# Performance work log

Measured on AMD Instinct MI355X. Metric: run time of the kernel, lower is better.

## Reference

```python
import jax, jax.numpy as jnp
import numpy as np

EPS = 1e-6

def _ln(x):
    mu = jnp.mean(x, -1, keepdims=True)
    var = jnp.mean((x - mu) ** 2, -1, keepdims=True)
    return (x - mu) / jnp.sqrt(var + EPS)

def _mha(q_in, k_in, v_in, w, mask, h):
    # w: [4, d, d] = (Wq, Wk, Wv, Wo), stored as [in, out]
    b, sq, d = q_in.shape
    dk = d // h
    q = (q_in @ w[0]).reshape(b, sq, h, dk)
    k = (k_in @ w[1]).reshape(b, k_in.shape[1], h, dk)
    v = (v_in @ w[2]).reshape(b, v_in.shape[1], h, dk)
    scores = jnp.einsum('bqhd,bkhd->bhqk', q, k) / np.sqrt(dk).astype(q.dtype)
    if mask is not None:
        scores = jnp.where(mask, scores, jnp.asarray(-jnp.inf, scores.dtype))
    attn = jax.nn.softmax(scores, -1)
    out = jnp.einsum('bhqk,bkhd->bqhd', attn, v).reshape(b, sq, d)
    return out @ w[3]

def setup_inputs() -> dict:
    B, S, D, V, NL, ML = 8, 256, 1024, 32000, 6, 256
    ks = jax.random.split(jax.random.key(0), 8)
    sc = 0.02
    return {
        'memory': jax.random.normal(ks[0], (B, S, D), jnp.float32),
        'gold_tokens': jax.random.randint(ks[1], (B, ML), 0, V),
        'attn_w': jax.random.normal(ks[2], (NL, 2, 4, D, D), jnp.float32) * sc,
        'ffn_w1': jax.random.normal(ks[3], (NL, D, 4 * D), jnp.float32) * sc,
        'ffn_w2': jax.random.normal(ks[4], (NL, 4 * D, D), jnp.float32) * sc,
        'tok_emb': jax.random.normal(ks[5], (V, D - ML), jnp.float32) * sc,
        'sos': jax.random.normal(ks[6], (D,), jnp.float32),
        'gen_w': jax.random.normal(ks[7], (D, V), jnp.float32) * sc,
    }

def reference(memory, gold_tokens, attn_w, ffn_w1, ffn_w2, tok_emb, sos, gen_w):
    B = memory.shape[0]
    ML = gold_tokens.shape[1]          # max_length == decoder len
    NL = attn_w.shape[0]
    H = 8
    temperature = 1.0
    # embedding: token embed (dim d-ML) concat one-hot position (dim ML)
    dec_input = gold_tokens[:, :-1]                      # [B, ML-1]
    tok = tok_emb[dec_input]                             # [B, ML-1, D-ML]
    pos = jax.nn.one_hot(jnp.arange(ML - 1), ML, dtype=tok.dtype)  # [ML-1, ML]
    pos = jnp.broadcast_to(pos[None], (B, ML - 1, ML))
    emb = jnp.concatenate([tok, pos], -1)                # [B, ML-1, D]
    sos_tok = jnp.broadcast_to(sos[None, None, :], (B, 1, sos.shape[0]))
    x = jnp.concatenate([sos_tok, emb], 1)               # [B, ML, D]
    causal = jnp.tril(jnp.ones((ML, ML), bool))[None, None]  # True = keep
    for l in range(NL):
        h1 = _ln(x)
        x = x + _mha(h1, h1, h1, attn_w[l, 0], causal, H)       # self-attn
        x = x + _mha(_ln(x), memory, memory, attn_w[l, 1], None, H)  # cross-attn (raw memory keys/values)
        h2 = _ln(x)
        x = x + jax.nn.relu(h2 @ ffn_w1[l]) @ ffn_w2[l]
    logits = _ln(x) @ gen_w
    return jax.nn.log_softmax(logits / temperature, -1)
```

## Files before the change

### kernel.cpp

```cpp
#include <hip/hip_runtime.h>
#include <hip/hip_bf16.h>
#include <cstdint>
#include <cstddef>

using bf16 = __hip_bfloat16;
typedef __attribute__((ext_vector_type(8))) short bf16x8;
typedef __attribute__((ext_vector_type(4))) float f32x4;

#define DEV static __device__ __forceinline__

DEV unsigned short f2bf(float f) {
    bf16 h = __float2bfloat16(f);
    return __builtin_bit_cast(unsigned short, h);
}

typedef const __attribute__((address_space(1))) void* as1cv;
typedef __attribute__((address_space(3))) void* as3v;

DEV void load_lds16(const void* g, void* l) {
    __builtin_amdgcn_global_load_lds((as1cv)g, (as3v)l, 16, 0, 0);
}

template<int EPI>
__global__ __launch_bounds__(256)
void gemm_k(const bf16* __restrict__ Ag, const bf16* __restrict__ Bg,
            void* __restrict__ Cg,
            int Mdim, int Ndim, int Kdim,
            int lda, int ldb, int ldc,
            int Hdim, long aZ1, long aZ2, long bZ1, long bZ2,
            long cZ1, long cZ2, float scale,
            float* __restrict__ pp, const bf16* __restrict__ Ag2, int ySplitA)
{
    __shared__ __align__(16) char lds[65536];

    const int t = threadIdx.x;
    const int wave = t >> 6, lane = t & 63;
    const int wr = wave >> 1, wc = wave & 1;
    const int lo = lane & 15, hi = lane >> 4;

    const int bx2 = blockIdx.x, by2 = blockIdx.y;
    const int m0 = bx2 * 128, n0 = by2 * 128;
    const int z = blockIdx.z;
    const int z1 = z / Hdim, z2 = z - z1 * Hdim;

    const bf16* Abase = (by2 >= ySplitA) ? Ag2 : Ag;
    const bf16* A = Abase + (size_t)z1 * aZ1 + (size_t)z2 * aZ2;
    const bf16* B = Bg + (size_t)z1 * bZ1 + (size_t)z2 * bZ2;

    f32x4 acc[4][4];
#pragma unroll
    for (int m = 0; m < 4; ++m)
#pragma unroll
        for (int n = 0; n < 4; ++n)
            acc[m][n] = f32x4{0.f, 0.f, 0.f, 0.f};

    const int nk = Kdim >> 6;

    auto stage = [&](int kt, int buf) {
        const int k0 = kt << 6;
        char* dA = lds + buf * 32768;
        char* dB = dA + 16384;
#pragma unroll
        for (int i = 0; i < 4; ++i) {
            int u = i * 256 + t;
            int row = u >> 3;
            int cb = (u & 7) ^ (row & 7);
            load_lds16(A + (size_t)(m0 + row) * lda + (k0 + cb * 8),
                       dA + i * 4096 + wave * 1024);
        }
#pragma unroll
        for (int i = 0; i < 4; ++i) {
            int u = i * 256 + t;
            int row = u >> 3;
            int cb = (u & 7) ^ (row & 7);
            load_lds16(B + (size_t)(n0 + row) * ldb + (k0 + cb * 8),
                       dB + i * 4096 + wave * 1024);
        }
    };

    stage(0, 0);
    int cur = 0;
    for (int kt = 0; kt < nk; ++kt) {
        __syncthreads();
        if (kt + 1 < nk) stage(kt + 1, cur ^ 1);
        char* ldsA = lds + cur * 32768;
        char* ldsB = ldsA + 16384;
#pragma unroll
        for (int kk = 0; kk < 2; ++kk) {
            bf16x8 af[4], bfr[4];
#pragma unroll
            for (int m = 0; m < 4; ++m) {
                int row = wr * 64 + m * 16 + lo;
                int cbyte = ((kk << 6) + (hi << 4)) ^ ((row & 7) << 4);
                af[m] = *(const bf16x8*)(ldsA + row * 128 + cbyte);
            }
#pragma unroll
            for (int n = 0; n < 4; ++n) {
                int row = wc * 64 + n * 16 + lo;
                int cbyte = ((kk << 6) + (hi << 4)) ^ ((row & 7) << 4);
                bfr[n] = *(const bf16x8*)(ldsB + row * 128 + cbyte);
            }
#pragma unroll
            for (int m = 0; m < 4; ++m)
#pragma unroll
                for (int n = 0; n < 4; ++n)
                    acc[m][n] = __builtin_amdgcn_mfma_f32_16x16x32_bf16(
                        af[m], bfr[n], acc[m][n], 0, 0, 0);
        }
        cur ^= 1;
    }

    const int rb = hi << 2;
    if (EPI == 0 || EPI == 1) {
        unsigned short* C = (unsigned short*)Cg + (size_t)z1 * cZ1 + (size_t)z2 * cZ2;
#pragma unroll
        for (int m = 0; m < 4; ++m)
#pragma unroll
            for (int n = 0; n < 4; ++n)
#pragma unroll
                for (int r = 0; r < 4; ++r) {
                    int row = m0 + wr * 64 + m * 16 + rb + r;
                    int col = n0 + wc * 64 + n * 16 + lo;
                    float v = acc[m][n][r];
                    if (EPI == 1) v = fmaxf(v, 0.f);
                    C[(size_t)row * ldc + col] = f2bf(v);
                }
    } else {
        float* C = (float*)Cg + (size_t)z1 * cZ1 + (size_t)z2 * cZ2;
#pragma unroll
        for (int m = 0; m < 4; ++m)
#pragma unroll
            for (int n = 0; n < 4; ++n)
#pragma unroll
                for (int r = 0; r < 4; ++r) {
                    int row = m0 + wr * 64 + m * 16 + rb + r;
                    int col = n0 + wc * 64 + n * 16 + lo;
                    atomicAdd(&C[(size_t)row * ldc + col], acc[m][n][r]);
                }
    }
}

__global__ __launch_bounds__(512, 2)
void gemm256_k(const bf16* __restrict__ Ag, const bf16* __restrict__ Bg,
               float* __restrict__ Cg, int Kdim, int lda, int ldb, int ldc,
               float* __restrict__ pp)
{
    __shared__ __align__(16) char lds[98304];

    const int t = threadIdx.x;
    const int wave = t >> 6, lane = t & 63;
    const int wr = wave >> 2, wc = wave & 3;
    const int lo = lane & 15, hi = lane >> 4;
    const int m0 = blockIdx.x * 256, n0 = blockIdx.y * 256;

    f32x4 acc[8][4];
#pragma unroll
    for (int m = 0; m < 8; ++m)
#pragma unroll
        for (int n = 0; n < 4; ++n)
            acc[m][n] = f32x4{0.f, 0.f, 0.f, 0.f};

    const int NT = Kdim >> 5;

    auto stageOp = [&](const bf16* Op, int ld, int base0, int kt, char* dst) {
#pragma unroll
        for (int i = 0; i < 2; ++i) {
            int u = i * 512 + t;
            int row = u >> 2, j = u & 3;
            int cb = j ^ (row & 3);
            load_lds16(Op + (size_t)(base0 + row) * ld + (kt << 5) + cb * 8,
                       dst + i * 8192 + wave * 1024);
        }
    };

    stageOp(Ag, lda, m0, 0, lds);
    stageOp(Bg, ldb, n0, 0, lds + 16384);
    stageOp(Ag, lda, m0, 1, lds + 32768);
    stageOp(Bg, ldb, n0, 1, lds + 32768 + 16384);

    for (int kt = 0; kt < NT; ++kt) {
        if (kt == NT - 1) asm volatile("s_waitcnt vmcnt(0)" ::: "memory");
        else              asm volatile("s_waitcnt vmcnt(4)" ::: "memory");
        __builtin_amdgcn_s_barrier();
        __builtin_amdgcn_sched_barrier(0);

        char* cA = lds + (kt % 3) * 32768;
        char* cB = cA + 16384;
        char* nA = lds + ((kt + 2) % 3) * 32768;

        if (kt + 2 < NT) stageOp(Ag, lda, m0, kt + 2, nA);
        bf16x8 bfr[4];
#pragma unroll
        for (int nf = 0; nf < 4; ++nf) {
            int rb_ = wc * 64 + nf * 16 + lo;
            bfr[nf] = *(const bf16x8*)(cB + rb_ * 64 + ((hi ^ (rb_ & 3)) << 4));
        }
        bf16x8 af[4];
#pragma unroll
        for (int mm = 0; mm < 4; ++mm) {
            int ra = wr * 128 + mm * 16 + lo;
            af[mm] = *(const bf16x8*)(cA + ra * 64 + ((hi ^ (ra & 3)) << 4));
        }
        __builtin_amdgcn_s_setprio(1);
#pragma unroll
        for (int mm = 0; mm < 4; ++mm)
#pragma unroll
            for (int nf = 0; nf < 4; ++nf)
                acc[mm][nf] = __builtin_amdgcn_mfma_f32_16x16x32_bf16(
                    af[mm], bfr[nf], acc[mm][nf], 0, 0, 0);
        __builtin_amdgcn_s_setprio(0);

        if (kt + 2 < NT) stageOp(Bg, ldb, n0, kt + 2, nA + 16384);
#pragma unroll
        for (int mm = 0; mm < 4; ++mm) {
            int ra = wr * 128 + (4 + mm) * 16 + lo;
            af[mm] = *(const bf16x8*)(cA + ra * 64 + ((hi ^ (ra & 3)) << 4));
        }
        __builtin_amdgcn_s_setprio(1);
#pragma unroll
        for (int mm = 0; mm < 4; ++mm)
#pragma unroll
            for (int nf = 0; nf < 4; ++nf)
                acc[4 + mm][nf] = __builtin_amdgcn_mfma_f32_16x16x32_bf16(
                    af[mm], bfr[nf], acc[4 + mm][nf], 0, 0, 0);
        __builtin_amdgcn_s_setprio(0);
    }

#pragma unroll
    for (int mf = 0; mf < 8; ++mf)
#pragma unroll
        for (int nf = 0; nf < 4; ++nf)
#pragma unroll
            for (int r = 0; r < 4; ++r) {
                int row = m0 + wr * 128 + mf * 16 + hi * 4 + r;
                int col = n0 + wc * 64 + nf * 16 + lo;
                __builtin_nontemporal_store(acc[mf][nf][r],
                                            &Cg[(size_t)row * ldc + col]);
            }
    __syncthreads();
    float* lp = (float*)lds;
#pragma unroll
    for (int mf = 0; mf < 8; ++mf)
#pragma unroll
        for (int r = 0; r < 4; ++r) {
            float vm = fmaxf(fmaxf(acc[mf][0][r], acc[mf][1][r]),
                             fmaxf(acc[mf][2][r], acc[mf][3][r]));
#pragma unroll
            for (int o = 1; o < 16; o <<= 1) vm = fmaxf(vm, __shfl_xor(vm, o));
            float vs = 0.f;
#pragma unroll
            for (int nf = 0; nf < 4; ++nf) vs += __expf(acc[mf][nf][r] - vm);
#pragma unroll
            for (int o = 1; o < 16; o <<= 1) vs += __shfl_xor(vs, o);
            if (lo == 0) {
                int rl = wr * 128 + mf * 16 + hi * 4 + r;
                lp[(rl * 4 + wc) * 2 + 0] = vm;
                lp[(rl * 4 + wc) * 2 + 1] = vs;
            }
        }
    __syncthreads();
    if (t < 256) {
        float mm = -3.4e38f, ss = 0.f;
#pragma unroll
        for (int w2 = 0; w2 < 4; ++w2) {
            float m2 = lp[(t * 4 + w2) * 2], s2 = lp[(t * 4 + w2) * 2 + 1];
            float nm = fmaxf(mm, m2);
            ss = ss * __expf(mm - nm) + s2 * __expf(m2 - nm);
            mm = nm;
        }
        size_t idx2 = ((size_t)(m0 + t) * gridDim.y + blockIdx.y) * 2;
        pp[idx2] = mm; pp[idx2 + 1] = ss;
    }
}

template<int CAUSAL>
__global__ __launch_bounds__(256)
void attn_k(const bf16* __restrict__ qkv, const bf16* __restrict__ VT,
            bf16* __restrict__ attno)
{
    __shared__ __align__(16) char ldsK[2][16384];
    __shared__ __align__(16) char ldsP[8192];
    const float SC = 0.088388347648318447f;

    const int t = threadIdx.x, w = t >> 6, lane = t & 63;
    const int lo = lane & 15, hi = lane >> 4;
    const int qb = blockIdx.x, z = blockIdx.y;
    const int b = z >> 3, h = z & 7;
    const int qr0 = qb * 64 + w * 16;

    const unsigned short* Qg = (const unsigned short*)qkv + (size_t)(b * 256) * 3072 + h * 128;
    const unsigned short* Kg = Qg + 1024;
    const unsigned short* VTz = (const unsigned short*)VT + (size_t)z * 32768;

    bf16x8 qf[4];
#pragma unroll
    for (int ks = 0; ks < 4; ++ks)
        qf[ks] = *(const bf16x8*)(Qg + (size_t)(qr0 + lo) * 3072 + ks * 32 + hi * 8);

    f32x4 accO[8];
#pragma unroll
    for (int n2 = 0; n2 < 8; ++n2) accO[n2] = f32x4{0.f, 0.f, 0.f, 0.f};
    float mrun[4], lrun[4];
#pragma unroll
    for (int r = 0; r < 4; ++r) { mrun[r] = -3.0e38f; lrun[r] = 0.f; }

    auto stageK = [&](int kt, int buf) {
#pragma unroll
        for (int i = 0; i < 4; ++i) {
            int u = i * 256 + t;
            int row = u >> 4, j = u & 15;
            int sj = (j & 8) | ((j ^ row) & 7);
            load_lds16(Kg + (size_t)(kt * 64 + row) * 3072 + sj * 8,
                       ldsK[buf] + i * 4096 + w * 1024);
        }
    };

    const int nkt = CAUSAL ? (qb + 1) : 4;
    stageK(0, 0);
    int cur = 0;
    for (int kt = 0; kt < nkt; ++kt) {
        __syncthreads();
        if (kt + 1 < nkt) stageK(kt + 1, cur ^ 1);

        f32x4 s4[4];
#pragma unroll
        for (int n = 0; n < 4; ++n) s4[n] = f32x4{0.f, 0.f, 0.f, 0.f};
#pragma unroll
        for (int ks = 0; ks < 4; ++ks)
#pragma unroll
            for (int n = 0; n < 4; ++n) {
                int kr = n * 16 + lo;
                int c = ks * 4 + hi;
                int sc2 = (c & 8) | ((c ^ (kr & 7)) & 7);
                bf16x8 kf = *(const bf16x8*)(ldsK[cur] + kr * 256 + sc2 * 16);
                s4[n] = __builtin_amdgcn_mfma_f32_16x16x32_bf16(qf[ks], kf, s4[n], 0, 0, 0);
            }

        float sv[4][4];
#pragma unroll
        for (int n = 0; n < 4; ++n)
#pragma unroll
            for (int r = 0; r < 4; ++r) {
                float v = s4[n][r] * SC;
                if (CAUSAL) {
                    int kg = kt * 64 + n * 16 + lo;
                    int qg2 = qb * 64 + w * 16 + hi * 4 + r;
                    if (kg > qg2) v = -3.0e38f;
                }
                sv[n][r] = v;
            }

        float sfv[4];
#pragma unroll
        for (int r = 0; r < 4; ++r) {
            float m2 = fmaxf(fmaxf(sv[0][r], sv[1][r]), fmaxf(sv[2][r], sv[3][r]));
#pragma unroll
            for (int o = 1; o < 16; o <<= 1) m2 = fmaxf(m2, __shfl_xor(m2, o));
            float mn = fmaxf(mrun[r], m2);
            sfv[r] = __expf(mrun[r] - mn);
            mrun[r] = mn;
        }
        float p[4][4], ts[4];
#pragma unroll
        for (int r = 0; r < 4; ++r) ts[r] = 0.f;
#pragma unroll
        for (int n = 0; n < 4; ++n)
#pragma unroll
            for (int r = 0; r < 4; ++r) {
                float e = __expf(sv[n][r] - mrun[r]);
                p[n][r] = e; ts[r] += e;
            }
#pragma unroll
        for (int r = 0; r < 4; ++r) {
            float s2 = ts[r];
#pragma unroll
            for (int o = 1; o < 16; o <<= 1) s2 += __shfl_xor(s2, o);
            lrun[r] = lrun[r] * sfv[r] + s2;
        }
#pragma unroll
        for (int n2 = 0; n2 < 8; ++n2)
#pragma unroll
            for (int r = 0; r < 4; ++r) accO[n2][r] *= sfv[r];

        char* pb = ldsP + w * 2048;
#pragma unroll
        for (int n = 0; n < 4; ++n)
#pragma unroll
            for (int r = 0; r < 4; ++r) {
                int q = hi * 4 + r, k = n * 16 + lo;
                int ch = (k >> 3) ^ (q & 7);
                *(unsigned short*)(pb + q * 128 + ch * 16 + (k & 7) * 2) = f2bf(p[n][r]);
            }

#pragma unroll
        for (int ks2 = 0; ks2 < 2; ++ks2) {
            int c2 = (ks2 * 4 + hi) ^ (lo & 7);
            bf16x8 pa = *(const bf16x8*)(pb + lo * 128 + c2 * 16);
#pragma unroll
            for (int n2 = 0; n2 < 8; ++n2) {
                int d = n2 * 16 + lo;
                bf16x8 vb = *(const bf16x8*)(VTz + (size_t)d * 256 + kt * 64 + ks2 * 32 + hi * 8);
                accO[n2] = __builtin_amdgcn_mfma_f32_16x16x32_bf16(pa, vb, accO[n2], 0, 0, 0);
            }
        }
        cur ^= 1;
    }

    float inv[4];
#pragma unroll
    for (int r = 0; r < 4; ++r) inv[r] = 1.f / lrun[r];
    unsigned short* Og = (unsigned short*)attno;
#pragma unroll
    for (int n2 = 0; n2 < 8; ++n2)
#pragma unroll
        for (int r = 0; r < 4; ++r) {
            int qg2 = qb * 64 + w * 16 + hi * 4 + r;
            int d = n2 * 16 + lo;
            Og[(size_t)(b * 256 + qg2) * 1024 + h * 128 + d] = f2bf(accO[n2][r] * inv[r]);
        }
}

DEV void wconv_tile(const float* __restrict__ W, unsigned short* __restrict__ WT,
                    int K, int N, int k0, int n0, int t, unsigned short* lds)
{
#pragma unroll
    for (int i = 0; i < 16; ++i) {
        int lin = i * 256 + t;
        int r = lin >> 6, c = lin & 63;
        float v = __builtin_nontemporal_load(&W[(size_t)(k0 + r) * N + n0 + c]);
        lds[c * 65 + r] = f2bf(v);
    }
    __syncthreads();
#pragma unroll
    for (int i = 0; i < 16; ++i) {
        int lin = i * 256 + t;
        int r = lin >> 6, c = lin & 63;
        WT[(size_t)(n0 + r) * K + k0 + c] = lds[r * 65 + c];
    }
}

__global__ __launch_bounds__(256)
void wconv_k(const float* __restrict__ W, bf16* __restrict__ WT, int K, int N)
{
    __shared__ unsigned short lds[64 * 65];
    size_t moff = (size_t)blockIdx.z * K * N;
    wconv_tile(W + moff, (unsigned short*)WT + moff, K, N,
               blockIdx.x * 64, blockIdx.y * 64, threadIdx.x, lds);
}

__global__ __launch_bounds__(256)
void wconv3_k(const float* __restrict__ Wa, const float* __restrict__ W1,
              const float* __restrict__ W2, bf16* __restrict__ WTa,
              bf16* __restrict__ WT1, bf16* __restrict__ WT2)
{
    __shared__ unsigned short lds[64 * 65];
    int bid = blockIdx.x, t = threadIdx.x;
    if (bid < 2048) {
        int mat = bid >> 8, r = bid & 255;
        size_t moff = (size_t)mat * 1048576;
        wconv_tile(Wa + moff, (unsigned short*)WTa + moff, 1024, 1024,
                   (r & 15) * 64, (r >> 4) * 64, t, lds);
    } else if (bid < 3072) {
        int idx = bid - 2048;
        wconv_tile(W1, (unsigned short*)WT1, 1024, 4096,
                   (idx & 15) * 64, (idx >> 4) * 64, t, lds);
    } else {
        int idx = bid - 3072;
        wconv_tile(W2, (unsigned short*)WT2, 4096, 1024,
                   (idx & 63) * 64, (idx >> 6) * 64, t, lds);
    }
}

__global__ __launch_bounds__(256)
void f2b_k(const float* __restrict__ in, bf16* __restrict__ out, int n4)
{
    int i = blockIdx.x * 256 + threadIdx.x;
    if (i >= n4) return;
    float4 v = ((const float4*)in)[i];
    ushort4 o;
    o.x = f2bf(v.x); o.y = f2bf(v.y); o.z = f2bf(v.z); o.w = f2bf(v.w);
    ((ushort4*)out)[i] = o;
}

__global__ __launch_bounds__(256)
void embed_k(const float* __restrict__ tok_emb, const int* __restrict__ gold,
             const float* __restrict__ sos, float* __restrict__ x)
{
    int row = blockIdx.x;
    int b = row >> 8, sq = row & 255;
    int c4 = threadIdx.x;
    float4 v;
    if (sq == 0) {
        v = ((const float4*)sos)[c4];
    } else {
        int c = c4 << 2;
        if (c < 768) {
            int tok = gold[b * 256 + sq - 1];
            v = ((const float4*)(tok_emb + (size_t)tok * 768))[c4];
        } else {
            int p = sq - 1;
            v.x = (c + 0 - 768 == p) ? 1.f : 0.f;
            v.y = (c + 1 - 768 == p) ? 1.f : 0.f;
            v.z = (c + 2 - 768 == p) ? 1.f : 0.f;
            v.w = (c + 3 - 768 == p) ? 1.f : 0.f;
        }
    }
    ((float4*)(x + (size_t)row * 1024))[c4] = v;
}

__global__ __launch_bounds__(256)
void ln_k(const float* __restrict__ x, bf16* __restrict__ out)
{
    int row = blockIdx.x;
    const float4* xr = (const float4*)(x + (size_t)row * 1024);
    float4 v = xr[threadIdx.x];
    float s = v.x + v.y + v.z + v.w;
    float ss = v.x * v.x + v.y * v.y + v.z * v.z + v.w * v.w;
    for (int o = 32; o > 0; o >>= 1) { s += __shfl_down(s, o); ss += __shfl_down(ss, o); }
    __shared__ float buf[8];
    int wv = threadIdx.x >> 6;
    if ((threadIdx.x & 63) == 0) { buf[wv] = s; buf[4 + wv] = ss; }
    __syncthreads();
    float S = buf[0] + buf[1] + buf[2] + buf[3];
    float SS = buf[4] + buf[5] + buf[6] + buf[7];
    float mean = S * (1.f / 1024.f);
    float var = SS * (1.f / 1024.f) - mean * mean;
    float rstd = rsqrtf(var + 1e-6f);
    ushort4 o;
    o.x = f2bf((v.x - mean) * rstd);
    o.y = f2bf((v.y - mean) * rstd);
    o.z = f2bf((v.z - mean) * rstd);
    o.w = f2bf((v.w - mean) * rstd);
    ((ushort4*)out)[(size_t)row * 256 + threadIdx.x] = o;
}

__global__ __launch_bounds__(256)
void vtrans_k(const bf16* __restrict__ v, bf16* __restrict__ VT)
{
    __shared__ unsigned short lds[128 * 65];
    int z = blockIdx.y;
    int b = z >> 3, hh = z & 7;
    int sc = blockIdx.x;
    const unsigned short* src = (const unsigned short*)v
        + (size_t)(b * 256 + sc * 64) * 3072 + hh * 128;
    int t = threadIdx.x;
#pragma unroll
    for (int i = 0; i < 32; ++i) {
        int lin = i * 256 + t;
        int sl = lin >> 7, d = lin & 127;
        lds[d * 65 + sl] = src[(size_t)sl * 3072 + d];
    }
    __syncthreads();
    unsigned short* dst = (unsigned short*)VT + (size_t)z * 32768 + sc * 64;
#pragma unroll
    for (int i = 0; i < 32; ++i) {
        int lin = i * 256 + t;
        int d = lin >> 6, sl = lin & 63;
        dst[(size_t)d * 256 + sl] = lds[d * 65 + sl];
    }
}

__global__ __launch_bounds__(256)
void lsesub_k(float* __restrict__ out, const float* __restrict__ pp)
{
    const int NB = 125;
    int row = blockIdx.x, t = threadIdx.x;
    float m = -3.4e38f, s = 0.f;
    if (t < NB) {
        m = pp[((size_t)row * NB + t) * 2];
        s = pp[((size_t)row * NB + t) * 2 + 1];
    }
    for (int o = 32; o > 0; o >>= 1) {
        float om = __shfl_down(m, o), os = __shfl_down(s, o);
        float nm = fmaxf(m, om);
        s = s * __expf(m - nm) + os * __expf(om - nm);
        m = nm;
    }
    __shared__ float bm[4], bs[4];
    __shared__ float sL;
    int wv = t >> 6;
    if ((t & 63) == 0) { bm[wv] = m; bs[wv] = s; }
    __syncthreads();
    if (t == 0) {
        float M = fmaxf(fmaxf(bm[0], bm[1]), fmaxf(bm[2], bm[3]));
        float S = bs[0] * __expf(bm[0] - M) + bs[1] * __expf(bm[1] - M)
                + bs[2] * __expf(bm[2] - M) + bs[3] * __expf(bm[3] - M);
        sL = M + logf(S);
    }
    __syncthreads();
    float L = sL;
    f32x4* p = (f32x4*)(out + (size_t)row * 32000);
    for (int i = t; i < 8000; i += 256) {
        f32x4 v = __builtin_nontemporal_load(&p[i]);
        v[0] -= L; v[1] -= L; v[2] -= L; v[3] -= L;
        __builtin_nontemporal_store(v, &p[i]);
    }
}

extern "C" void kernel_launch(void* const* d_in, const int* in_sizes, int n_in,
                              void* d_out, int out_size, void* d_ws, size_t ws_size,
                              hipStream_t stream)
{
    (void)in_sizes; (void)n_in; (void)out_size;
    const float* memory  = (const float*)d_in[0];
    const int*   gold    = (const int*)d_in[1];
    const float* attn_w  = (const float*)d_in[2];
    const float* ffn_w1  = (const float*)d_in[3];
    const float* ffn_w2  = (const float*)d_in[4];
    const float* tok_emb = (const float*)d_in[5];
    const float* sos     = (const float*)d_in[6];
    const float* gen_w   = (const float*)d_in[7];
    float* out = (float*)d_out;

    char* ws = (char*)d_ws;
    const size_t o_attnW = 0;
    const size_t o_ffn1W = o_attnW + 16777216;
    const size_t o_ffn2W = o_ffn1W + 8388608;
    const size_t o_qkv   = o_ffn2W + 8388608;
    const size_t o_attno = o_qkv + 12582912;
    const size_t o_tmp   = o_attno + 4194304;
    const size_t o_mem   = o_tmp + 29360128;
    const size_t o_x     = o_mem + 4194304;
    const size_t o_h     = o_x + 8388608;
    const size_t o_lse   = o_h + 4194304;
    const size_t NEEDED  = o_lse + 8192;
    if (ws_size < NEEDED) return;

    bf16*  attnWT = (bf16*)(ws + o_attnW);
    bf16*  ffn1WT = (bf16*)(ws + o_ffn1W);
    bf16*  ffn2WT = (bf16*)(ws + o_ffn2W);
    bf16*  qkv    = (bf16*)(ws + o_qkv);
    bf16*  attno  = (bf16*)(ws + o_attno);
    bf16*  VT     = (bf16*)(ws + o_tmp + 25165824);
    bf16*  ffnmid = (bf16*)(ws + o_tmp);
    bf16*  memb   = (bf16*)(ws + o_mem);
    float* x      = (float*)(ws + o_x);
    bf16*  h      = (bf16*)(ws + o_h);
    float* parts  = (float*)(ws + o_mem);
    bf16*  genWT  = (bf16*)(ws + 0);

    const int BIG = 1 << 30;

    f2b_k<<<2048, 256, 0, stream>>>(memory, memb, 2048 * 1024 / 4);
    embed_k<<<2048, 256, 0, stream>>>(tok_emb, gold, sos, x);

    for (int l = 0; l < 6; ++l) {
        wconv3_k<<<4096, 256, 0, stream>>>(attn_w + (size_t)l * 8388608,
            ffn_w1 + (size_t)l * 4194304, ffn_w2 + (size_t)l * 4194304,
            attnWT, ffn1WT, ffn2WT);

        ln_k<<<2048, 256, 0, stream>>>(x, h);
        gemm_k<0><<<dim3(16,24,1), 256, 0, stream>>>(h, attnWT, qkv,
            2048, 3072, 1024, 1024, 1024, 3072, 1, 0,0,0,0,0,0, 0.f, nullptr, nullptr, BIG);
        vtrans_k<<<dim3(4,64), 256, 0, stream>>>(qkv + 2048, VT);
        attn_k<1><<<dim3(4,64), 256, 0, stream>>>(qkv, VT, attno);
        gemm_k<5><<<dim3(16,8,2), 256, 0, stream>>>(attno, attnWT + 3 * 1048576, x,
            2048, 1024, 512, 1024, 1024, 1024, 2, 0,512, 0,512, 0,0, 0.f, nullptr, nullptr, BIG);

        ln_k<<<2048, 256, 0, stream>>>(x, h);
        gemm_k<0><<<dim3(16,24,1), 256, 0, stream>>>(h, attnWT + 4 * 1048576, qkv,
            2048, 3072, 1024, 1024, 1024, 3072, 1, 0,0,0,0,0,0, 0.f, nullptr, memb, 8);
        vtrans_k<<<dim3(4,64), 256, 0, stream>>>(qkv + 2048, VT);
        attn_k<0><<<dim3(4,64), 256, 0, stream>>>(qkv, VT, attno);
        gemm_k<5><<<dim3(16,8,2), 256, 0, stream>>>(attno, attnWT + 7 * 1048576, x,
            2048, 1024, 512, 1024, 1024, 1024, 2, 0,512, 0,512, 0,0, 0.f, nullptr, nullptr, BIG);

        ln_k<<<2048, 256, 0, stream>>>(x, h);
        gemm_k<1><<<dim3(16,32,1), 256, 0, stream>>>(h, ffn1WT, ffnmid,
            2048, 4096, 1024, 1024, 1024, 4096, 1, 0,0,0,0,0,0, 0.f, nullptr, nullptr, BIG);
        gemm_k<5><<<dim3(16,8,4), 256, 0, stream>>>(ffnmid, ffn2WT, x,
            2048, 1024, 1024, 4096, 4096, 1024, 4, 0,1024, 0,1024, 0,0, 0.f, nullptr, nullptr, BIG);
    }

    wconv_k<<<dim3(16,500,1), 256, 0, stream>>>(gen_w, genWT, 1024, 32000);
    ln_k<<<2048, 256, 0, stream>>>(x, h);
    gemm256_k<<<dim3(8,125), 512, 0, stream>>>(h, genWT, out, 1024, 1024, 1024, 32000, parts);
    lsesub_k<<<2048, 256, 0, stream>>>(out, parts);
}
```

Before: 1.667 ms.

## Single-buffer generic GEMM and reshape vocab GEMM tile to 512x128

The generic gemm_k drops its double-buffered LDS pipeline for a single buffer with load-sync-compute-sync, halving its shared memory so more blocks can be resident per CU. The vocab projection GEMM moves from 256x256 tiles to 512x128 tiles on a 4x250 grid, with a new swizzle, larger LDS and no min-blocks hint. The partial log-sum-exp bookkeeping is updated to 2 waves per row and 250 column blocks. The cost is losing load/compute overlap in every layer GEMM, and the vocab kernel now risks lower occupancy.

```diff
diff --git a/kernel.cpp b/kernel.cpp
--- a/kernel.cpp
+++ b/kernel.cpp
@@ -31,7 +31,9 @@
             long cZ1, long cZ2, float scale,
             float* __restrict__ pp, const bf16* __restrict__ Ag2, int ySplitA)
 {
-    __shared__ __align__(16) char lds[65536];
+    __shared__ __align__(16) char lds[32768];
+    char* ldsA = lds;
+    char* ldsB = lds + 16384;
 
     const int t = threadIdx.x;
     const int wave = t >> 6, lane = t & 63;
@@ -55,18 +57,15 @@
             acc[m][n] = f32x4{0.f, 0.f, 0.f, 0.f};
 
     const int nk = Kdim >> 6;
-
-    auto stage = [&](int kt, int buf) {
+    for (int kt = 0; kt < nk; ++kt) {
         const int k0 = kt << 6;
-        char* dA = lds + buf * 32768;
-        char* dB = dA + 16384;
 #pragma unroll
         for (int i = 0; i < 4; ++i) {
             int u = i * 256 + t;
             int row = u >> 3;
             int cb = (u & 7) ^ (row & 7);
             load_lds16(A + (size_t)(m0 + row) * lda + (k0 + cb * 8),
-                       dA + i * 4096 + wave * 1024);
+                       ldsA + i * 4096 + wave * 1024);
         }
 #pragma unroll
         for (int i = 0; i < 4; ++i) {
@@ -74,17 +73,9 @@
             int row = u >> 3;
             int cb = (u & 7) ^ (row & 7);
             load_lds16(B + (size_t)(n0 + row) * ldb + (k0 + cb * 8),
-                       dB + i * 4096 + wave * 1024);
-        }
-    };
-
-    stage(0, 0);
-    int cur = 0;
-    for (int kt = 0; kt < nk; ++kt) {
+                       ldsB + i * 4096 + wave * 1024);
+        }
         __syncthreads();
-        if (kt + 1 < nk) stage(kt + 1, cur ^ 1);
-        char* ldsA = lds + cur * 32768;
-        char* ldsB = ldsA + 16384;
 #pragma unroll
         for (int kk = 0; kk < 2; ++kk) {
             bf16x8 af[4], bfr[4];
@@ -107,7 +98,7 @@
                     acc[m][n] = __builtin_amdgcn_mfma_f32_16x16x32_bf16(
                         af[m], bfr[n], acc[m][n], 0, 0, 0);
         }
-        cur ^= 1;
+        __syncthreads();
     }
 
     const int rb = hi << 2;
@@ -140,18 +131,18 @@
     }
 }
 
-__global__ __launch_bounds__(512, 2)
+__global__ __launch_bounds__(512)
 void gemm256_k(const bf16* __restrict__ Ag, const bf16* __restrict__ Bg,
                float* __restrict__ Cg, int Kdim, int lda, int ldb, int ldc,
                float* __restrict__ pp)
 {
-    __shared__ __align__(16) char lds[98304];
+    __shared__ __align__(16) char lds[122880];
 
     const int t = threadIdx.x;
     const int wave = t >> 6, lane = t & 63;
-    const int wr = wave >> 2, wc = wave & 3;
+    const int wr = wave >> 1, wc = wave & 1;
     const int lo = lane & 15, hi = lane >> 4;
-    const int m0 = blockIdx.x * 256, n0 = blockIdx.y * 256;
+    const int m0 = blockIdx.x * 512, n0 = blockIdx.y * 128;
 
     f32x4 acc[8][4];
 #pragma unroll
@@ -162,44 +153,48 @@
 
     const int NT = Kdim >> 5;
 
-    auto stageOp = [&](const bf16* Op, int ld, int base0, int kt, char* dst) {
-#pragma unroll
-        for (int i = 0; i < 2; ++i) {
+    auto stageA = [&](int kt, char* dst) {
+#pragma unroll
+        for (int i = 0; i < 4; ++i) {
             int u = i * 512 + t;
             int row = u >> 2, j = u & 3;
-            int cb = j ^ (row & 3);
-            load_lds16(Op + (size_t)(base0 + row) * ld + (kt << 5) + cb * 8,
+            int cb = j ^ ((row >> 1) & 3);
+            load_lds16(Ag + (size_t)(m0 + row) * lda + (kt << 5) + cb * 8,
                        dst + i * 8192 + wave * 1024);
         }
     };
-
-    stageOp(Ag, lda, m0, 0, lds);
-    stageOp(Bg, ldb, n0, 0, lds + 16384);
-    stageOp(Ag, lda, m0, 1, lds + 32768);
-    stageOp(Bg, ldb, n0, 1, lds + 32768 + 16384);
+    auto stageB = [&](int kt, char* dst) {
+        int row = t >> 2, j = t & 3;
+        int cb = j ^ ((row >> 1) & 3);
+        load_lds16(Bg + (size_t)(n0 + row) * ldb + (kt << 5) + cb * 8,
+                   dst + wave * 1024);
+    };
+
+    stageA(0, lds);             stageB(0, lds + 32768);
+    stageA(1, lds + 40960);     stageB(1, lds + 40960 + 32768);
 
     for (int kt = 0; kt < NT; ++kt) {
         if (kt == NT - 1) asm volatile("s_waitcnt vmcnt(0)" ::: "memory");
-        else              asm volatile("s_waitcnt vmcnt(4)" ::: "memory");
+        else              asm volatile("s_waitcnt vmcnt(5)" ::: "memory");
         __builtin_amdgcn_s_barrier();
         __builtin_amdgcn_sched_barrier(0);
 
-        char* cA = lds + (kt % 3) * 32768;
-        char* cB = cA + 16384;
-        char* nA = lds + ((kt + 2) % 3) * 32768;
-
-        if (kt + 2 < NT) stageOp(Ag, lda, m0, kt + 2, nA);
+        char* cA = lds + (kt % 3) * 40960;
+        char* cB = cA + 32768;
+        char* nA = lds + ((kt + 2) % 3) * 40960;
+
+        if (kt + 2 < NT) stageA(kt + 2, nA);
         bf16x8 bfr[4];
 #pragma unroll
         for (int nf = 0; nf < 4; ++nf) {
             int rb_ = wc * 64 + nf * 16 + lo;
-            bfr[nf] = *(const bf16x8*)(cB + rb_ * 64 + ((hi ^ (rb_ & 3)) << 4));
+            bfr[nf] = *(const bf16x8*)(cB + rb_ * 64 + ((hi ^ ((rb_ >> 1) & 3)) << 4));
         }
         bf16x8 af[4];
 #pragma unroll
         for (int mm = 0; mm < 4; ++mm) {
             int ra = wr * 128 + mm * 16 + lo;
-            af[mm] = *(const bf16x8*)(cA + ra * 64 + ((hi ^ (ra & 3)) << 4));
+            af[mm] = *(const bf16x8*)(cA + ra * 64 + ((hi ^ ((ra >> 1) & 3)) << 4));
         }
         __builtin_amdgcn_s_setprio(1);
 #pragma unroll
@@ -210,11 +205,11 @@
                     af[mm], bfr[nf], acc[mm][nf], 0, 0, 0);
         __builtin_amdgcn_s_setprio(0);
 
-        if (kt + 2 < NT) stageOp(Bg, ldb, n0, kt + 2, nA + 16384);
+        if (kt + 2 < NT) stageB(kt + 2, nA + 32768);
 #pragma unroll
         for (int mm = 0; mm < 4; ++mm) {
             int ra = wr * 128 + (4 + mm) * 16 + lo;
-            af[mm] = *(const bf16x8*)(cA + ra * 64 + ((hi ^ (ra & 3)) << 4));
+            af[mm] = *(const bf16x8*)(cA + ra * 64 + ((hi ^ ((ra >> 1) & 3)) << 4));
         }
         __builtin_amdgcn_s_setprio(1);
 #pragma unroll
@@ -254,20 +249,16 @@
             for (int o = 1; o < 16; o <<= 1) vs += __shfl_xor(vs, o);
             if (lo == 0) {
                 int rl = wr * 128 + mf * 16 + hi * 4 + r;
-                lp[(rl * 4 + wc) * 2 + 0] = vm;
-                lp[(rl * 4 + wc) * 2 + 1] = vs;
+                lp[(rl * 2 + wc) * 2 + 0] = vm;
+                lp[(rl * 2 + wc) * 2 + 1] = vs;
             }
         }
     __syncthreads();
-    if (t < 256) {
-        float mm = -3.4e38f, ss = 0.f;
-#pragma unroll
-        for (int w2 = 0; w2 < 4; ++w2) {
-            float m2 = lp[(t * 4 + w2) * 2], s2 = lp[(t * 4 + w2) * 2 + 1];
-            float nm = fmaxf(mm, m2);
-            ss = ss * __expf(mm - nm) + s2 * __expf(m2 - nm);
-            mm = nm;
-        }
+    {
+        float ma = lp[(t * 2 + 0) * 2], sa = lp[(t * 2 + 0) * 2 + 1];
+        float mb = lp[(t * 2 + 1) * 2], sb = lp[(t * 2 + 1) * 2 + 1];
+        float mm = fmaxf(ma, mb);
+        float ss = sa * __expf(ma - mm) + sb * __expf(mb - mm);
         size_t idx2 = ((size_t)(m0 + t) * gridDim.y + blockIdx.y) * 2;
         pp[idx2] = mm; pp[idx2 + 1] = ss;
     }
@@ -563,7 +554,7 @@
 __global__ __launch_bounds__(256)
 void lsesub_k(float* __restrict__ out, const float* __restrict__ pp)
 {
-    const int NB = 125;
+    const int NB = 250;
     int row = blockIdx.x, t = threadIdx.x;
     float m = -3.4e38f, s = 0.f;
     if (t < NB) {
@@ -674,6 +665,6 @@
 
     wconv_k<<<dim3(16,500,1), 256, 0, stream>>>(gen_w, genWT, 1024, 32000);
     ln_k<<<2048, 256, 0, stream>>>(x, h);
-    gemm256_k<<<dim3(8,125), 512, 0, stream>>>(h, genWT, out, 1024, 1024, 1024, 32000, parts);
+    gemm256_k<<<dim3(4,250), 512, 0, stream>>>(h, genWT, out, 1024, 1024, 1024, 32000, parts);
     lsesub_k<<<2048, 256, 0, stream>>>(out, parts);
 }
```

Result: slower. 1.784 ms (+7.0%).
